# Kernel optimization log

Measured on AMD Instinct MI355X. Metric: run time of the kernel, lower is better.

The kernel has to match this reference:

```python
import jax, jax.numpy as jnp
import numpy as np

EPS = 1e-8

def setup_inputs() -> dict:
    key = jax.random.key(0)
    k1, k2, k3 = jax.random.split(key, 3)
    B, N, L = 4096, 8192, 256
    logits = jax.random.normal(k1, (B, N), dtype=jnp.float32)
    positive_ids = jax.random.randint(k2, (B, L), 0, N, dtype=jnp.int64)
    positive_weights = jax.random.uniform(k3, (B, L), dtype=jnp.float32)
    return {"logits": logits, "positive_ids": positive_ids, "positive_weights": positive_weights}

def reference(logits, positive_ids, positive_weights):
    # gather positive logits: [B, L]
    gathered = jnp.take_along_axis(logits, positive_ids, axis=1)
    w = positive_weights.astype(jnp.float32)
    w = w / jnp.maximum(w.sum(axis=-1, keepdims=True), EPS)
    # sort by weight descending
    order = jnp.argsort(-w, axis=-1)
    ordered_logits = jnp.take_along_axis(gathered, order, axis=1)
    ordered_weights = jnp.take_along_axis(w, order, axis=1)
    # suffix logsumexp in one reverse cumulative pass: [B, L]
    suffix_lse = jax.lax.cumlogsumexp(ordered_logits, axis=1, reverse=True)
    listmle = jnp.sum(ordered_weights * (suffix_lse - ordered_logits), axis=-1)
    return jnp.mean(listmle)
```

## Files before the change

kernel.cpp:

```cpp
#include <hip/hip_runtime.h>
#include <hip/hip_bf16.h>
#include <math.h>

#define BROWS 4096
#define NCOLS 8192
#define LLEN  256
#define EPSV  1e-8f

__global__ __launch_bounds__(256) void listmle_kernel(
    const float* __restrict__ logits,
    const int*   __restrict__ ids,
    const float* __restrict__ weights,
    float*       __restrict__ partial)
{
    __shared__ float    s_g[LLEN];
    __shared__ float    s_w[LLEN];
    __shared__ unsigned s_key[2][LLEN];
    __shared__ float    s_aggs[4];
    __shared__ float    s_redt[4], s_redw[4];

    const int tid  = threadIdx.x;
    const int lane = tid & 63;
    const int wv   = tid >> 6;
    const int b    = blockIdx.x;

    int   id = ids[(size_t)b * LLEN + tid];
    float w  = weights[(size_t)b * LLEN + tid];
    float g  = logits[(size_t)b * NCOLS + id];

    unsigned key = (__float_as_uint(w) & 0xFFFFFF00u) | (unsigned)(LLEN - 1 - tid);

    #pragma unroll
    for (int k = 2; k <= 64; k <<= 1) {
        #pragma unroll
        for (int j = k >> 1; j > 0; j >>= 1) {
            const bool keep_max = (((tid & k) == 0) == ((tid & j) == 0));
            unsigned p  = __shfl_xor(key, j);
            unsigned mx = key > p ? key : p;
            unsigned mn = key > p ? p : key;
            key = keep_max ? mx : mn;
        }
    }

    s_g[tid] = g;
    s_w[tid] = w;

    int phase = 0;
    #pragma unroll
    for (int k = 128; k <= LLEN; k <<= 1) {
        #pragma unroll
        for (int j = k >> 1; j > 0; j >>= 1) {
            const bool keep_max = (((tid & k) == 0) == ((tid & j) == 0));
            unsigned p;
            if (j >= 64) {
                s_key[phase][tid] = key;
                __syncthreads();
                p = s_key[phase][tid ^ j];
                phase ^= 1;
            } else {
                p = __shfl_xor(key, j);
            }
            unsigned mx = key > p ? key : p;
            unsigned mn = key > p ? p : key;
            key = keep_max ? mx : mn;
        }
    }

    const int pos = (LLEN - 1) - (int)(key & 0xFFu);
    const float ow = s_w[pos];
    const float og = s_g[pos];

    float s = __expf(og);
    #pragma unroll
    for (int off = 1; off < 64; off <<= 1) {
        float sp = __shfl_down(s, off);
        if (lane + off < 64) s += sp;
    }
    if (lane == 0) s_aggs[wv] = s;
    __syncthreads();
    float T = 0.0f;
    #pragma unroll
    for (int w2 = 0; w2 < 4; ++w2)
        if (w2 > wv) T += s_aggs[w2];
    const float suffix_lse = __logf(s + T);

    float t  = ow * (suffix_lse - og);
    float ws = ow;
    #pragma unroll
    for (int o = 32; o > 0; o >>= 1) {
        t  += __shfl_down(t, o);
        ws += __shfl_down(ws, o);
    }
    if (lane == 0) { s_redt[wv] = t; s_redw[wv] = ws; }
    __syncthreads();
    if (tid == 0) {
        float tot  = s_redt[0] + s_redt[1] + s_redt[2] + s_redt[3];
        float wsum = s_redw[0] + s_redw[1] + s_redw[2] + s_redw[3];
        partial[b] = tot / fmaxf(wsum, EPSV);
    }
}

__global__ __launch_bounds__(256) void reduce_kernel(
    const float* __restrict__ partial, float* __restrict__ out)
{
    __shared__ float s_red[4];
    const int tid  = threadIdx.x;
    const int lane = tid & 63;
    const int wv   = tid >> 6;

    float v = 0.0f;
    #pragma unroll
    for (int i = 0; i < BROWS / 256; ++i)
        v += partial[i * 256 + tid];

    #pragma unroll
    for (int o = 32; o > 0; o >>= 1) v += __shfl_down(v, o);
    if (lane == 0) s_red[wv] = v;
    __syncthreads();
    if (tid == 0)
        out[0] = (s_red[0] + s_red[1] + s_red[2] + s_red[3]) * (1.0f / (float)BROWS);
}

extern "C" void kernel_launch(void* const* d_in, const int* in_sizes, int n_in,
                              void* d_out, int out_size, void* d_ws, size_t ws_size,
                              hipStream_t stream) {
    const float* logits  = (const float*)d_in[0];
    const int*   ids     = (const int*)d_in[1];
    const float* weights = (const float*)d_in[2];
    float* out     = (float*)d_out;
    float* partial = (float*)d_ws;

    listmle_kernel<<<dim3(BROWS), dim3(LLEN), 0, stream>>>(logits, ids, weights, partial);
    reduce_kernel<<<dim3(1), dim3(256), 0, stream>>>(partial, out);
}
```

Before: 189.0 us.

## Process one row per wavefront with four elements per lane

Assigns each 256-element row to a single 64-lane wavefront, four rows per block. Each lane holds four elements, so the bitonic sort runs entirely in registers and wave shuffles and the block-wide __syncthreads stages disappear. The suffix sum becomes a per-lane local scan plus a wave scan. Loads of ids and weights are vectorised to 128 bits. In exchange each lane does more serial work and holds more registers, and there is less thread-level parallelism hiding the latency of the random logits gathers.

```diff
diff --git a/kernel.cpp b/kernel.cpp
--- a/kernel.cpp
+++ b/kernel.cpp
@@ -1,11 +1,17 @@
 #include <hip/hip_runtime.h>
-#include <hip/hip_bf16.h>
 #include <math.h>
 
 #define BROWS 4096
 #define NCOLS 8192
 #define LLEN  256
 #define EPSV  1e-8f
+#define RPB   4
+
+#define CMPEX(x, y, xmax) {                         \
+    unsigned _mx = (x) > (y) ? (x) : (y);           \
+    unsigned _mn = (x) > (y) ? (y) : (x);           \
+    (x) = (xmax) ? _mx : _mn;                       \
+    (y) = (xmax) ? _mn : _mx; }
 
 __global__ __launch_bounds__(256) void listmle_kernel(
     const float* __restrict__ logits,
@@ -13,91 +19,100 @@
     const float* __restrict__ weights,
     float*       __restrict__ partial)
 {
-    __shared__ float    s_g[LLEN];
-    __shared__ float    s_w[LLEN];
-    __shared__ unsigned s_key[2][LLEN];
-    __shared__ float    s_aggs[4];
-    __shared__ float    s_redt[4], s_redw[4];
+    __shared__ float2 s_gw[RPB][LLEN];
 
     const int tid  = threadIdx.x;
     const int lane = tid & 63;
     const int wv   = tid >> 6;
-    const int b    = blockIdx.x;
+    const int row  = blockIdx.x * RPB + wv;
 
-    int   id = ids[(size_t)b * LLEN + tid];
-    float w  = weights[(size_t)b * LLEN + tid];
-    float g  = logits[(size_t)b * NCOLS + id];
+    const int4   id4 = reinterpret_cast<const int4*>(ids + (size_t)row * LLEN)[lane];
+    const float4 w4  = reinterpret_cast<const float4*>(weights + (size_t)row * LLEN)[lane];
+    const float* lrow = logits + (size_t)row * NCOLS;
 
-    unsigned key = (__float_as_uint(w) & 0xFFFFFF00u) | (unsigned)(LLEN - 1 - tid);
+    float g0 = lrow[id4.x];
+    float g1 = lrow[id4.y];
+    float g2 = lrow[id4.z];
+    float g3 = lrow[id4.w];
+
+    const int e0 = lane << 2;
+    unsigned k0 = (__float_as_uint(w4.x) & 0xFFFFFF00u) | (unsigned)(255 - (e0 + 0));
+    unsigned k1 = (__float_as_uint(w4.y) & 0xFFFFFF00u) | (unsigned)(255 - (e0 + 1));
+    unsigned k2 = (__float_as_uint(w4.z) & 0xFFFFFF00u) | (unsigned)(255 - (e0 + 2));
+    unsigned k3 = (__float_as_uint(w4.w) & 0xFFFFFF00u) | (unsigned)(255 - (e0 + 3));
 
     #pragma unroll
-    for (int k = 2; k <= 64; k <<= 1) {
+    for (int k = 2; k <= 256; k <<= 1) {
         #pragma unroll
         for (int j = k >> 1; j > 0; j >>= 1) {
-            const bool keep_max = (((tid & k) == 0) == ((tid & j) == 0));
-            unsigned p  = __shfl_xor(key, j);
-            unsigned mx = key > p ? key : p;
-            unsigned mn = key > p ? p : key;
-            key = keep_max ? mx : mn;
+            if (j >= 4) {
+                const int  lj = j >> 2;
+                const bool km = (((e0 & k) == 0) == ((e0 & j) == 0));
+                unsigned p0 = __shfl_xor(k0, lj);
+                unsigned p1 = __shfl_xor(k1, lj);
+                unsigned p2 = __shfl_xor(k2, lj);
+                unsigned p3 = __shfl_xor(k3, lj);
+                { unsigned mx = k0 > p0 ? k0 : p0, mn = k0 > p0 ? p0 : k0; k0 = km ? mx : mn; }
+                { unsigned mx = k1 > p1 ? k1 : p1, mn = k1 > p1 ? p1 : k1; k1 = km ? mx : mn; }
+                { unsigned mx = k2 > p2 ? k2 : p2, mn = k2 > p2 ? p2 : k2; k2 = km ? mx : mn; }
+                { unsigned mx = k3 > p3 ? k3 : p3, mn = k3 > p3 ? p3 : k3; k3 = km ? mx : mn; }
+            } else if (j == 2) {
+                const bool km = ((e0 & k) == 0);
+                CMPEX(k0, k2, km);
+                CMPEX(k1, k3, km);
+            } else {
+                bool km01, km23;
+                if (k == 2) { km01 = true; km23 = false; }
+                else        { km01 = km23 = ((e0 & k) == 0); }
+                CMPEX(k0, k1, km01);
+                CMPEX(k2, k3, km23);
+            }
         }
     }
 
-    s_g[tid] = g;
-    s_w[tid] = w;
+    float2* sw = s_gw[wv];
+    reinterpret_cast<float4*>(sw)[lane * 2 + 0] = make_float4(g0, w4.x, g1, w4.y);
+    reinterpret_cast<float4*>(sw)[lane * 2 + 1] = make_float4(g2, w4.z, g3, w4.w);
+    __builtin_amdgcn_wave_barrier();
 
-    int phase = 0;
-    #pragma unroll
-    for (int k = 128; k <= LLEN; k <<= 1) {
-        #pragma unroll
-        for (int j = k >> 1; j > 0; j >>= 1) {
-            const bool keep_max = (((tid & k) == 0) == ((tid & j) == 0));
-            unsigned p;
-            if (j >= 64) {
-                s_key[phase][tid] = key;
-                __syncthreads();
-                p = s_key[phase][tid ^ j];
-                phase ^= 1;
-            } else {
-                p = __shfl_xor(key, j);
-            }
-            unsigned mx = key > p ? key : p;
-            unsigned mn = key > p ? p : key;
-            key = keep_max ? mx : mn;
-        }
-    }
+    const int p0i = 255 - (int)(k0 & 0xFFu);
+    const int p1i = 255 - (int)(k1 & 0xFFu);
+    const int p2i = 255 - (int)(k2 & 0xFFu);
+    const int p3i = 255 - (int)(k3 & 0xFFu);
+    const float2 gw0 = sw[p0i];
+    const float2 gw1 = sw[p1i];
+    const float2 gw2 = sw[p2i];
+    const float2 gw3 = sw[p3i];
 
-    const int pos = (LLEN - 1) - (int)(key & 0xFFu);
-    const float ow = s_w[pos];
-    const float og = s_g[pos];
+    const float x0 = __expf(gw0.x);
+    const float x1 = __expf(gw1.x);
+    const float x2 = __expf(gw2.x);
+    const float x3 = __expf(gw3.x);
 
-    float s = __expf(og);
+    const float lt = x0 + x1 + x2 + x3;
+    float S = lt;
     #pragma unroll
     for (int off = 1; off < 64; off <<= 1) {
-        float sp = __shfl_down(s, off);
-        if (lane + off < 64) s += sp;
+        float sp = __shfl_down(S, off);
+        if (lane + off < 64) S += sp;
     }
-    if (lane == 0) s_aggs[wv] = s;
-    __syncthreads();
-    float T = 0.0f;
+    const float tail = S - lt;
+    const float s3 = x3 + tail;
+    const float s2 = x2 + s3;
+    const float s1 = x1 + s2;
+    const float s0 = x0 + s1;
+
+    float t  = gw0.y * (__logf(s0) - gw0.x)
+             + gw1.y * (__logf(s1) - gw1.x)
+             + gw2.y * (__logf(s2) - gw2.x)
+             + gw3.y * (__logf(s3) - gw3.x);
+    float ws = gw0.y + gw1.y + gw2.y + gw3.y;
     #pragma unroll
-    for (int w2 = 0; w2 < 4; ++w2)
-        if (w2 > wv) T += s_aggs[w2];
-    const float suffix_lse = __logf(s + T);
-
-    float t  = ow * (suffix_lse - og);
-    float ws = ow;
-    #pragma unroll
-    for (int o = 32; o > 0; o >>= 1) {
-        t  += __shfl_down(t, o);
-        ws += __shfl_down(ws, o);
+    for (int off = 32; off > 0; off >>= 1) {
+        t  += __shfl_down(t, off);
+        ws += __shfl_down(ws, off);
     }
-    if (lane == 0) { s_redt[wv] = t; s_redw[wv] = ws; }
-    __syncthreads();
-    if (tid == 0) {
-        float tot  = s_redt[0] + s_redt[1] + s_redt[2] + s_redt[3];
-        float wsum = s_redw[0] + s_redw[1] + s_redw[2] + s_redw[3];
-        partial[b] = tot / fmaxf(wsum, EPSV);
-    }
+    if (lane == 0) partial[row] = t / fmaxf(ws, EPSV);
 }
 
 __global__ __launch_bounds__(256) void reduce_kernel(
@@ -130,6 +145,6 @@
     float* out     = (float*)d_out;
     float* partial = (float*)d_ws;
 
-    listmle_kernel<<<dim3(BROWS), dim3(LLEN), 0, stream>>>(logits, ids, weights, partial);
+    listmle_kernel<<<dim3(BROWS / RPB), dim3(256), 0, stream>>>(logits, ids, weights, partial);
     reduce_kernel<<<dim3(1), dim3(256), 0, stream>>>(partial, out);
 }
```

Result: no change. 187.2 us (-1.0%).
